# Kernel tuning notes

Hardware: AMD Instinct MI355X
Metric: run time of the kernel (lower is better)

The kernel has to match this reference:

```python
import jax, jax.numpy as jnp
import numpy as np

N_POOL = 8  # init kwarg n

def setup_inputs() -> dict:
    key = jax.random.key(0)
    k1, k2 = jax.random.split(key)
    B, H, W, C = 8, 256, 512, 16
    FIL = 16  # must equal C for the final subtract to be shape-valid
    feature_map = jax.random.normal(k1, (B, H, W, C), dtype=jnp.float32)
    kernel = jax.random.normal(k2, (5, 5, C, FIL), dtype=jnp.float32) * 0.05  # HWIO
    bias = jnp.zeros((FIL,), dtype=jnp.float32)
    return {"feature_map": feature_map, "kernel": kernel, "bias": bias}


def _inpaint_rows(x, kernel_masked, bias):
    # x: [B, h, w, C]. Original builds, per output row r, a 5-row stack
    # [padded[r], 0, 0, 0, padded[r+4]] and runs a 5x5 valid conv.
    # Since rows 1..3 of the stack are zero, this equals a single 5x5 valid
    # conv over the zero-padded input with kernel rows 1..3 zeroed out.
    xp = jnp.pad(x, ((0, 0), (2, 2), (2, 2), (0, 0)))
    y = jax.lax.conv_general_dilated(
        xp, kernel_masked, window_strides=(1, 1), padding='VALID',
        dimension_numbers=('NHWC', 'HWIO', 'NHWC'))
    return jax.nn.relu(y + bias)


def reference(feature_map, kernel, bias):
    B, H, W, C = feature_map.shape
    FIL = kernel.shape[-1]
    n = N_POOL
    ph = H // n  # pool size along H (SAME == VALID since H % ph == 0)
    w2 = W // 2
    # AveragePooling2D(pool=(H/n, 2), strides same)
    out = feature_map.reshape(B, n, ph, w2, 2, C).mean(axis=(2, 4))  # [B,n,w2,C]

    row_mask = jnp.array([1.0, 0.0, 0.0, 0.0, 1.0], dtype=kernel.dtype)
    kernel_masked = kernel * row_mask[:, None, None, None]

    row_op = _inpaint_rows(out, kernel_masked, bias)  # [B,n,w2,FIL]
    col_op = jnp.transpose(
        _inpaint_rows(jnp.transpose(out, (0, 2, 1, 3)), kernel_masked, bias),
        (0, 2, 1, 3))  # [B,n,w2,FIL]

    row_up = jax.image.resize(row_op, (B, H, W, FIL), method='bilinear')
    col_up = jax.image.resize(col_op, (B, H, W, FIL), method='bilinear')

    stacked_op = jnp.concatenate([row_up, col_up], axis=3)        # [B,H,W,2*FIL]
    stacked_orig = jnp.concatenate([feature_map, feature_map], axis=3)
    diff = stacked_orig - stacked_op
    return jnp.concatenate([feature_map, diff], axis=3)          # [B,H,W,3*C]
```

## Files before the change

kernel.cpp:

```cpp
#include <hip/hip_runtime.h>

#define B 8
#define H 256
#define W 512
#define C 16
#define FIL 16
#define NP 8
#define PH 32
#define W2 256
#define CH 8
#define POOL_ELEMS (B*NP*W2*C)

typedef float f32x4 __attribute__((ext_vector_type(4)));

__global__ __launch_bounds__(256) void pool_kernel(const float* __restrict__ fm,
                                                   float* __restrict__ P) {
    int blk = blockIdx.x;
    int ch = blk & (CH - 1);
    int bi = blk >> 3;
    int t = threadIdx.x;
    const float4* src = (const float4*)fm + (size_t)bi * (PH * W * C / 4) + ch * 256 + t;
    float4 acc = make_float4(0.f, 0.f, 0.f, 0.f);
#pragma unroll 8
    for (int hh = 0; hh < PH; ++hh) {
        float4 v = src[hh * (W * C / 4)];
        acc.x += v.x; acc.y += v.y; acc.z += v.z; acc.w += v.w;
    }
    __shared__ float4 s[256];
    s[t] = acc;
    __syncthreads();
    if (t < 128) {
        int u = t >> 2, q = t & 3;
        float4 a = s[u * 8 + q], b2 = s[u * 8 + 4 + q];
        float4 r = make_float4((a.x + b2.x) * (1.0f / 64.0f),
                               (a.y + b2.y) * (1.0f / 64.0f),
                               (a.z + b2.z) * (1.0f / 64.0f),
                               (a.w + b2.w) * (1.0f / 64.0f));
        float4* out = (float4*)(P + (size_t)bi * (W2 * C)) + ch * 128 + t;
        *out = r;
    }
}

__global__ __launch_bounds__(512) void conv_kernel(const float* __restrict__ P,
                                                   const float* __restrict__ kern,
                                                   const float* __restrict__ bias,
                                                   float* __restrict__ ROW,
                                                   float* __restrict__ COL) {
    int blk = blockIdx.x;
    int b = blk >> 3, i = blk & 7;
    int t = threadIdx.x;
    __shared__ float K0[5 * C * FIL];
    __shared__ float K4[5 * C * FIL];
    for (int idx = t; idx < 5 * C * FIL; idx += 512) {
        K0[idx] = kern[idx];
        K4[idx] = kern[4 * 5 * C * FIL + idx];
    }
    __syncthreads();
    int j = t & 255;
    const float* Pb = P + (size_t)b * (NP * W2 * C);
    float acc[FIL];
#pragma unroll
    for (int f = 0; f < FIL; ++f) acc[f] = bias[f];

    if (t < 256) {
#pragma unroll
        for (int rr = 0; rr < 2; ++rr) {
            int ii = i + (rr ? 2 : -2);
            if (ii < 0 || ii >= NP) continue;
            const float* Kr = rr ? K4 : K0;
            for (int s = 0; s < 5; ++s) {
                int jj = j + s - 2;
                if (jj < 0 || jj >= W2) continue;
                const float* p = Pb + (size_t)(ii * W2 + jj) * C;
                for (int c = 0; c < C; ++c) {
                    float pv = p[c];
                    const float* kk = Kr + (s * C + c) * FIL;
#pragma unroll
                    for (int f = 0; f < FIL; ++f) acc[f] = fmaf(pv, kk[f], acc[f]);
                }
            }
        }
        float* o = ROW + ((size_t)(b * NP + i) * W2 + j) * FIL;
#pragma unroll
        for (int f = 0; f < FIL; ++f) o[f] = fmaxf(acc[f], 0.0f);
    } else {
        for (int s = 0; s < 5; ++s) {
            int ii = i + s - 2;
            if (ii < 0 || ii >= NP) continue;
#pragma unroll
            for (int rr = 0; rr < 2; ++rr) {
                int jj = j + (rr ? 2 : -2);
                if (jj < 0 || jj >= W2) continue;
                const float* Kr = rr ? K4 : K0;
                const float* p = Pb + (size_t)(ii * W2 + jj) * C;
                for (int c = 0; c < C; ++c) {
                    float pv = p[c];
                    const float* kk = Kr + (s * C + c) * FIL;
#pragma unroll
                    for (int f = 0; f < FIL; ++f) acc[f] = fmaf(pv, kk[f], acc[f]);
                }
            }
        }
        float* o = COL + ((size_t)(b * NP + i) * W2 + j) * FIL;
#pragma unroll
        for (int f = 0; f < FIL; ++f) o[f] = fmaxf(acc[f], 0.0f);
    }
}

__global__ __launch_bounds__(256) void up_kernel(const float* __restrict__ fm,
                                                 const float* __restrict__ ROW,
                                                 const float* __restrict__ COL,
                                                 float* __restrict__ out) {
    int blk = blockIdx.x;
    int b = blk >> 8, h = blk & 255;
    int t = threadIdx.x;
    __shared__ float Rs[W2 * C];
    __shared__ float Cs[W2 * C];

    float sh = (h + 0.5f) * (1.0f / 32.0f) - 0.5f;
    float flh = floorf(sh);
    float fh = sh - flh;
    int i0 = (int)flh;
    int i1 = min(i0 + 1, NP - 1);
    i0 = max(i0, 0);
    float wa = 1.0f - fh, wb = fh;

    const float4* r0 = (const float4*)(ROW + (size_t)(b * NP + i0) * (W2 * C));
    const float4* r1 = (const float4*)(ROW + (size_t)(b * NP + i1) * (W2 * C));
    const float4* c0 = (const float4*)(COL + (size_t)(b * NP + i0) * (W2 * C));
    const float4* c1 = (const float4*)(COL + (size_t)(b * NP + i1) * (W2 * C));
#pragma unroll
    for (int k = 0; k < 4; ++k) {
        int idx = t + k * 256;
        float4 a = r0[idx], bv = r1[idx];
        ((float4*)Rs)[idx] = make_float4(wa * a.x + wb * bv.x, wa * a.y + wb * bv.y,
                                         wa * a.z + wb * bv.z, wa * a.w + wb * bv.w);
        float4 ca = c0[idx], cb = c1[idx];
        ((float4*)Cs)[idx] = make_float4(wa * ca.x + wb * cb.x, wa * ca.y + wb * cb.y,
                                         wa * ca.z + wb * cb.z, wa * ca.w + wb * cb.w);
    }
    __syncthreads();

    const float4* fmr = (const float4*)(fm + (size_t)(b * H + h) * (W * C));
    f32x4* orow = (f32x4*)(out + (size_t)(b * H + h) * (W * 48));
    for (int slot = t; slot < W * 12; slot += 256) {
        int p = slot / 12;
        int q = slot - p * 12;
        int cc = (q & 3) * 4;
        float4 v = fmr[p * 4 + (q & 3)];
        if (q >= 4) {
            float sw = 0.5f * p - 0.25f;
            float flw = floorf(sw);
            float fw = sw - flw;
            int j0i = max((int)flw, 0);
            int j1i = min((int)flw + 1, W2 - 1);
            const float* S = (q < 8) ? Rs : Cs;
            const float* A  = S + j0i * 16 + cc;
            const float* Bv = S + j1i * 16 + cc;
            float iw = 1.0f - fw;
            v.x -= iw * A[0] + fw * Bv[0];
            v.y -= iw * A[1] + fw * Bv[1];
            v.z -= iw * A[2] + fw * Bv[2];
            v.w -= iw * A[3] + fw * Bv[3];
        }
        f32x4 vv = { v.x, v.y, v.z, v.w };
        __builtin_nontemporal_store(vv, &orow[slot]);
    }
}

extern "C" void kernel_launch(void* const* d_in, const int* in_sizes, int n_in,
                              void* d_out, int out_size, void* d_ws, size_t ws_size,
                              hipStream_t stream) {
    const float* fm   = (const float*)d_in[0];
    const float* kern = (const float*)d_in[1];
    const float* bias = (const float*)d_in[2];
    float* out = (float*)d_out;
    float* P   = (float*)d_ws;
    float* ROW = P + POOL_ELEMS;
    float* COL = ROW + POOL_ELEMS;

    pool_kernel<<<B * NP * CH, 256, 0, stream>>>(fm, P);
    conv_kernel<<<B * NP, 512, 0, stream>>>(P, kern, bias, ROW, COL);
    up_kernel<<<B * H, 256, 0, stream>>>(fm, ROW, COL, out);
}
```

Baseline: 72.29 us.

## Split conv work across more blocks and make upsample loop trip count fixed

The conv kernel now launches four times as many 256-thread blocks, with each thread computing 8 of the 16 output filters and reading input channels as float4. With only 64 blocks before, the conv stage could not fill the GPU. The upsample kernel moves to 384 threads so each thread keeps a fixed (pixel, quad) slot across 16 unrolled iterations, which removes the per-iteration divide and branch setup. The cost is duplicated input loads across the two filter halves and more registers from the unrolling.

New measurement: 66.48 us. -8.0%, faster.

```diff
diff --git a/kernel.cpp b/kernel.cpp
--- a/kernel.cpp
+++ b/kernel.cpp
@@ -41,48 +41,59 @@
     }
 }
 
-__global__ __launch_bounds__(512) void conv_kernel(const float* __restrict__ P,
+__global__ __launch_bounds__(256) void conv_kernel(const float* __restrict__ P,
                                                    const float* __restrict__ kern,
                                                    const float* __restrict__ bias,
                                                    float* __restrict__ ROW,
                                                    float* __restrict__ COL) {
     int blk = blockIdx.x;
-    int b = blk >> 3, i = blk & 7;
+    int part = blk & 3;
+    int bi = blk >> 2;
+    int b = bi >> 3, i = bi & 7;
     int t = threadIdx.x;
     __shared__ float K0[5 * C * FIL];
     __shared__ float K4[5 * C * FIL];
-    for (int idx = t; idx < 5 * C * FIL; idx += 512) {
+    for (int idx = t; idx < 5 * C * FIL; idx += 256) {
         K0[idx] = kern[idx];
         K4[idx] = kern[4 * 5 * C * FIL + idx];
     }
     __syncthreads();
-    int j = t & 255;
+    bool is_row = (part < 2);
+    int jhalf = part & 1;
+    int j = jhalf * 128 + (t >> 1);
+    int fh = (t & 1) * 8;
     const float* Pb = P + (size_t)b * (NP * W2 * C);
-    float acc[FIL];
-#pragma unroll
-    for (int f = 0; f < FIL; ++f) acc[f] = bias[f];
-
-    if (t < 256) {
+    float acc[8];
+#pragma unroll
+    for (int f = 0; f < 8; ++f) acc[f] = bias[fh + f];
+
+    if (is_row) {
 #pragma unroll
         for (int rr = 0; rr < 2; ++rr) {
             int ii = i + (rr ? 2 : -2);
             if (ii < 0 || ii >= NP) continue;
-            const float* Kr = rr ? K4 : K0;
+            const float* Kr = (rr ? K4 : K0) + fh;
             for (int s = 0; s < 5; ++s) {
                 int jj = j + s - 2;
                 if (jj < 0 || jj >= W2) continue;
-                const float* p = Pb + (size_t)(ii * W2 + jj) * C;
-                for (int c = 0; c < C; ++c) {
-                    float pv = p[c];
-                    const float* kk = Kr + (s * C + c) * FIL;
-#pragma unroll
-                    for (int f = 0; f < FIL; ++f) acc[f] = fmaf(pv, kk[f], acc[f]);
+                const float4* p4 = (const float4*)(Pb + (size_t)(ii * W2 + jj) * C);
+#pragma unroll
+                for (int cq = 0; cq < 4; ++cq) {
+                    float4 pv = p4[cq];
+                    const float* kk = Kr + (s * C + cq * 4) * FIL;
+#pragma unroll
+                    for (int f = 0; f < 8; ++f) {
+                        acc[f] = fmaf(pv.x, kk[f], acc[f]);
+                        acc[f] = fmaf(pv.y, kk[FIL + f], acc[f]);
+                        acc[f] = fmaf(pv.z, kk[2 * FIL + f], acc[f]);
+                        acc[f] = fmaf(pv.w, kk[3 * FIL + f], acc[f]);
+                    }
                 }
             }
         }
-        float* o = ROW + ((size_t)(b * NP + i) * W2 + j) * FIL;
-#pragma unroll
-        for (int f = 0; f < FIL; ++f) o[f] = fmaxf(acc[f], 0.0f);
+        float* o = ROW + ((size_t)(b * NP + i) * W2 + j) * FIL + fh;
+#pragma unroll
+        for (int f = 0; f < 8; ++f) o[f] = fmaxf(acc[f], 0.0f);
     } else {
         for (int s = 0; s < 5; ++s) {
             int ii = i + s - 2;
@@ -91,23 +102,29 @@
             for (int rr = 0; rr < 2; ++rr) {
                 int jj = j + (rr ? 2 : -2);
                 if (jj < 0 || jj >= W2) continue;
-                const float* Kr = rr ? K4 : K0;
-                const float* p = Pb + (size_t)(ii * W2 + jj) * C;
-                for (int c = 0; c < C; ++c) {
-                    float pv = p[c];
-                    const float* kk = Kr + (s * C + c) * FIL;
-#pragma unroll
-                    for (int f = 0; f < FIL; ++f) acc[f] = fmaf(pv, kk[f], acc[f]);
+                const float* Kr = (rr ? K4 : K0) + fh;
+                const float4* p4 = (const float4*)(Pb + (size_t)(ii * W2 + jj) * C);
+#pragma unroll
+                for (int cq = 0; cq < 4; ++cq) {
+                    float4 pv = p4[cq];
+                    const float* kk = Kr + (s * C + cq * 4) * FIL;
+#pragma unroll
+                    for (int f = 0; f < 8; ++f) {
+                        acc[f] = fmaf(pv.x, kk[f], acc[f]);
+                        acc[f] = fmaf(pv.y, kk[FIL + f], acc[f]);
+                        acc[f] = fmaf(pv.z, kk[2 * FIL + f], acc[f]);
+                        acc[f] = fmaf(pv.w, kk[3 * FIL + f], acc[f]);
+                    }
                 }
             }
         }
-        float* o = COL + ((size_t)(b * NP + i) * W2 + j) * FIL;
-#pragma unroll
-        for (int f = 0; f < FIL; ++f) o[f] = fmaxf(acc[f], 0.0f);
-    }
-}
-
-__global__ __launch_bounds__(256) void up_kernel(const float* __restrict__ fm,
+        float* o = COL + ((size_t)(b * NP + i) * W2 + j) * FIL + fh;
+#pragma unroll
+        for (int f = 0; f < 8; ++f) o[f] = fmaxf(acc[f], 0.0f);
+    }
+}
+
+__global__ __launch_bounds__(384) void up_kernel(const float* __restrict__ fm,
                                                  const float* __restrict__ ROW,
                                                  const float* __restrict__ COL,
                                                  float* __restrict__ out) {
@@ -129,9 +146,7 @@
     const float4* r1 = (const float4*)(ROW + (size_t)(b * NP + i1) * (W2 * C));
     const float4* c0 = (const float4*)(COL + (size_t)(b * NP + i0) * (W2 * C));
     const float4* c1 = (const float4*)(COL + (size_t)(b * NP + i1) * (W2 * C));
-#pragma unroll
-    for (int k = 0; k < 4; ++k) {
-        int idx = t + k * 256;
+    for (int idx = t; idx < W2 * C / 4; idx += 384) {
         float4 a = r0[idx], bv = r1[idx];
         ((float4*)Rs)[idx] = make_float4(wa * a.x + wb * bv.x, wa * a.y + wb * bv.y,
                                          wa * a.z + wb * bv.z, wa * a.w + wb * bv.w);
@@ -141,20 +156,24 @@
     }
     __syncthreads();
 
+    int p_local = t / 12;
+    int q = t - p_local * 12;
+    int cc = (q & 3) * 4;
+    bool is_copy = (q < 4);
+    const float* S = (q < 8) ? Rs : Cs;
+
     const float4* fmr = (const float4*)(fm + (size_t)(b * H + h) * (W * C));
     f32x4* orow = (f32x4*)(out + (size_t)(b * H + h) * (W * 48));
-    for (int slot = t; slot < W * 12; slot += 256) {
-        int p = slot / 12;
-        int q = slot - p * 12;
-        int cc = (q & 3) * 4;
+#pragma unroll
+    for (int k = 0; k < 16; ++k) {
+        int p = k * 32 + p_local;
         float4 v = fmr[p * 4 + (q & 3)];
-        if (q >= 4) {
+        if (!is_copy) {
             float sw = 0.5f * p - 0.25f;
             float flw = floorf(sw);
             float fw = sw - flw;
             int j0i = max((int)flw, 0);
             int j1i = min((int)flw + 1, W2 - 1);
-            const float* S = (q < 8) ? Rs : Cs;
             const float* A  = S + j0i * 16 + cc;
             const float* Bv = S + j1i * 16 + cc;
             float iw = 1.0f - fw;
@@ -164,7 +183,7 @@
             v.w -= iw * A[3] + fw * Bv[3];
         }
         f32x4 vv = { v.x, v.y, v.z, v.w };
-        __builtin_nontemporal_store(vv, &orow[slot]);
+        __builtin_nontemporal_store(vv, &orow[(size_t)p * 12 + q]);
     }
 }
 
@@ -180,6 +199,6 @@
     float* COL = ROW + POOL_ELEMS;
 
     pool_kernel<<<B * NP * CH, 256, 0, stream>>>(fm, P);
-    conv_kernel<<<B * NP, 512, 0, stream>>>(P, kern, bias, ROW, COL);
-    up_kernel<<<B * H, 256, 0, stream>>>(fm, ROW, COL, out);
-}
+    conv_kernel<<<B * NP * 4, 256, 0, stream>>>(P, kern, bias, ROW, COL);
+    up_kernel<<<B * H, 384, 0, stream>>>(fm, ROW, COL, out);
+}
```
